# Optimization experiments

Measured on AMD Instinct MI355X. Metric: run time of the kernel, lower is better.

## Reference

```python
import jax, jax.numpy as jnp
import numpy as np

BN_EPS = 1e-5
NUM_ROUTING_ITERS = 3


def _bn(x, gamma, beta, axes):
    # training-mode batch norm (torch default train mode): batch statistics
    mean = x.mean(axes, keepdims=True)
    var = x.var(axes, keepdims=True)
    return (x - mean) * jax.lax.rsqrt(var + BN_EPS) * gamma + beta


def _squash(x):
    # squash over last dim: sn * x / ((1+sn) * sqrt(sn))
    sn = jnp.sum(x * x, axis=-1, keepdims=True)
    return sn * x / ((1.0 + sn) * jnp.sqrt(sn))


def setup_inputs() -> dict:
    key = jax.random.key(0)
    ks = jax.random.split(key, 16)
    B, N = 4, 2048          # batch, num_points
    P, Q = 1024, 16         # prim_caps_size, prim_vec_size
    L, V = 64, 64           # latent_caps_size, latent_vec_size
    OUT = 40
    s = 0.02
    return {
        "x": jax.random.normal(ks[0], (B, 3, N), dtype=jnp.float32),
        # ConvLayer
        "w1": jax.random.normal(ks[1], (64, 3), dtype=jnp.float32) * s,
        "b1": jnp.zeros((64,), jnp.float32),
        "g1": jnp.ones((64,), jnp.float32),
        "be1": jnp.zeros((64,), jnp.float32),
        "w2": jax.random.normal(ks[2], (128, 64), dtype=jnp.float32) * s,
        "b2": jnp.zeros((128,), jnp.float32),
        "g2": jnp.ones((128,), jnp.float32),
        "be2": jnp.zeros((128,), jnp.float32),
        # PrimaryPointCapsLayer: Q parallel conv1d(128->P, k=1)+BN branches, stacked
        "w3": jax.random.normal(ks[3], (Q, P, 128), dtype=jnp.float32) * s,
        "b3": jnp.zeros((Q, P), jnp.float32),
        "g3": jnp.ones((Q, P), jnp.float32),
        "be3": jnp.zeros((Q, P), jnp.float32),
        # LatentCapsLayer routing weights
        "Wr": jax.random.normal(ks[4], (L, P, V, Q), dtype=jnp.float32) * 0.01,
        # classifier head
        "fc_w": jax.random.normal(ks[5], (OUT, L * V), dtype=jnp.float32) * s,
        "fc_b": jnp.zeros((OUT,), jnp.float32),
    }


def reference(x, w1, b1, g1, be1, w2, b2, g2, be2, w3, b3, g3, be3, Wr, fc_w, fc_b):
    B = x.shape[0]
    # ConvLayer: two 1x1 conv1d + BN + ReLU
    h = jnp.einsum("oc,bcn->bon", w1, x) + b1[None, :, None]
    h = jax.nn.relu(_bn(h, g1[None, :, None], be1[None, :, None], (0, 2)))
    h = jnp.einsum("oc,bcn->bon", w2, h) + b2[None, :, None]
    h = jax.nn.relu(_bn(h, g2[None, :, None], be2[None, :, None], (0, 2)))  # [B,128,N]

    # PrimaryPointCapsLayer: Q branches of conv1d+BN+global maxpool, vectorized
    u = jnp.einsum("qpc,bcn->bqpn", w3, h) + b3[None, :, :, None]  # [B,Q,P,N]
    u = _bn(u, g3[None, :, :, None], be3[None, :, :, None], (0, 3))
    u = u.max(axis=-1)                      # global maxpool -> [B,Q,P]
    u = jnp.transpose(u, (0, 2, 1))         # stack dim=2 in torch -> [B,P,Q]
    u = _squash(u)                          # squash over prim_vec

    # LatentCapsLayer dynamic routing
    u_hat = jnp.einsum("lpvq,bpq->blpv", Wr, u)   # [B,L,P,V]
    u_hat_d = jax.lax.stop_gradient(u_hat)
    L, P = Wr.shape[0], Wr.shape[1]
    b_ij = jnp.zeros((B, L, P), u_hat.dtype)
    for _ in range(NUM_ROUTING_ITERS - 1):
        c_ij = jax.nn.softmax(b_ij, axis=1)
        v_j = _squash(jnp.einsum("blp,blpv->blv", c_ij, u_hat_d))
        b_ij = b_ij + jnp.einsum("blv,blpv->blp", v_j, u_hat_d)
    c_ij = jax.nn.softmax(b_ij, axis=1)
    v_j = _squash(jnp.einsum("blp,blpv->blv", c_ij, u_hat))  # [B,L,V]

    presence = jnp.linalg.norm(v_j, axis=2)                   # [B,L]
    logits = v_j.reshape(B, -1) @ fc_w.T + fc_b               # [B,OUT]
    return (logits, presence)
```

## Files before the change

kernel.cpp:

```cpp
#include <hip/hip_runtime.h>
#include <math.h>

#define BN_EPS 1e-5f

typedef __attribute__((ext_vector_type(8))) _Float16 half8;
typedef __attribute__((ext_vector_type(4))) float f32x4;
#define SPLIT_S  2048.0f
#define INV_S    (1.0f/2048.0f)

__global__ void k_conv1(const float* __restrict__ x, const float* __restrict__ w1,
                        float* __restrict__ y1) {
    int i = blockIdx.x * 256 + threadIdx.x;
    int o = i >> 11;
    int bn4 = (i & 2047) * 4;
    int b = bn4 >> 11, n = bn4 & 2047;
    const float* xb = x + (size_t)b * 6144 + n;
    float4 x0 = *(const float4*)(xb);
    float4 x1 = *(const float4*)(xb + 2048);
    float4 x2 = *(const float4*)(xb + 4096);
    float wa = w1[o*3+0], wb = w1[o*3+1], wc = w1[o*3+2];
    float4 r;
    r.x = wa*x0.x + wb*x1.x + wc*x2.x;
    r.y = wa*x0.y + wb*x1.y + wc*x2.y;
    r.z = wa*x0.z + wb*x1.z + wc*x2.z;
    r.w = wa*x0.w + wb*x1.w + wc*x2.w;
    *(float4*)(y1 + o * 8192 + bn4) = r;
}

__global__ void k_stats(const float* __restrict__ y, float* __restrict__ mean,
                        float* __restrict__ inv) {
    int c = blockIdx.x, t = threadIdx.x;
    float s = 0.f, ss = 0.f;
    const float4* src = (const float4*)(y + c * 8192);
    for (int i = t; i < 2048; i += 256) {
        float4 v = src[i];
        s += v.x + v.y + v.z + v.w;
        ss = fmaf(v.x, v.x, fmaf(v.y, v.y, fmaf(v.z, v.z, fmaf(v.w, v.w, ss))));
    }
    __shared__ float rs[256], rss[256];
    rs[t] = s; rss[t] = ss;
    __syncthreads();
    for (int off = 128; off > 0; off >>= 1) {
        if (t < off) { rs[t] += rs[t+off]; rss[t] += rss[t+off]; }
        __syncthreads();
    }
    if (t == 0) {
        float m = rs[0] * (1.f/8192.f);
        float var = rss[0] * (1.f/8192.f) - m*m;
        mean[c] = m;
        inv[c]  = rsqrtf(var + BN_EPS);
    }
}

__global__ void k_bnrelu(const float* __restrict__ y, float* __restrict__ h,
                         const float* __restrict__ mean, const float* __restrict__ inv,
                         const float* __restrict__ g, const float* __restrict__ be, int total4) {
    int i = blockIdx.x * 256 + threadIdx.x;
    if (i >= total4) return;
    int c = i >> 11;
    float sc = inv[c] * g[c], sh = be[c] - mean[c] * sc;
    float4 v = *(const float4*)(y + i * 4);
    v.x = fmaxf(fmaf(v.x, sc, sh), 0.f);
    v.y = fmaxf(fmaf(v.y, sc, sh), 0.f);
    v.z = fmaxf(fmaf(v.z, sc, sh), 0.f);
    v.w = fmaxf(fmaf(v.w, sc, sh), 0.f);
    *(float4*)(h + i * 4) = v;
}

__global__ __launch_bounds__(256) void k_conv2(const float* __restrict__ h1,
                                               const float* __restrict__ w2,
                                               float* __restrict__ y2) {
    int bn0 = (blockIdx.x * 256 + threadIdx.x) * 4;
    int og0 = blockIdx.y * 4;
    float4 acc[4];
#pragma unroll
    for (int j = 0; j < 4; ++j) acc[j] = float4{0.f,0.f,0.f,0.f};
    for (int c = 0; c < 64; ++c) {
        float4 hv = *(const float4*)(h1 + c*8192 + bn0);
#pragma unroll
        for (int j = 0; j < 4; ++j) {
            float w = w2[(og0+j)*64 + c];
            acc[j].x = fmaf(w, hv.x, acc[j].x); acc[j].y = fmaf(w, hv.y, acc[j].y);
            acc[j].z = fmaf(w, hv.z, acc[j].z); acc[j].w = fmaf(w, hv.w, acc[j].w);
        }
    }
#pragma unroll
    for (int j = 0; j < 4; ++j) *(float4*)(y2 + (og0+j)*8192 + bn0) = acc[j];
}

__global__ void k_split_w3(const float* __restrict__ w, _Float16* __restrict__ hi,
                           _Float16* __restrict__ lo) {
    int base = blockIdx.x * 256 + threadIdx.x;
#pragma unroll
    for (int it = 0; it < 4; ++it) {
        int i = (base + it * 131072) * 4;
        float4 d = *reinterpret_cast<const float4*>(w + i);
        float vs[4] = {d.x, d.y, d.z, d.w};
#pragma unroll
        for (int j = 0; j < 4; ++j) {
            _Float16 h = (_Float16)vs[j];
            hi[i + j] = h;
            lo[i + j] = (_Float16)((vs[j] - (float)h) * SPLIT_S);
        }
    }
}

__global__ __launch_bounds__(256) void k_h2t_split(const float* __restrict__ y2,
        const float* __restrict__ mean, const float* __restrict__ inv,
        const float* __restrict__ g, const float* __restrict__ be,
        _Float16* __restrict__ hi, _Float16* __restrict__ lo) {
    __shared__ float tile[64][65];
    const int t = threadIdx.x;
    const int bn0 = blockIdx.x * 64, c0 = blockIdx.y * 64;
#pragma unroll
    for (int r = 0; r < 16; ++r) {
        int idx = r * 256 + t;
        int cl = idx >> 6, bnl = idx & 63;
        int c = c0 + cl;
        float v = y2[(size_t)c * 8192 + bn0 + bnl];
        v = (v - mean[c]) * inv[c] * g[c] + be[c];
        tile[cl][bnl] = v > 0.f ? v : 0.f;
    }
    __syncthreads();
#pragma unroll
    for (int r = 0; r < 16; ++r) {
        int idx = r * 256 + t;
        int bnl = idx >> 6, cl = idx & 63;
        float v = tile[cl][bnl];
        _Float16 h = (_Float16)v;
        size_t o = (size_t)(bn0 + bnl) * 128 + c0 + cl;
        hi[o] = h;
        lo[o] = (_Float16)((v - (float)h) * SPLIT_S);
    }
}

__global__ __launch_bounds__(256, 2) void k_caps(
        const _Float16* __restrict__ w3h, const _Float16* __restrict__ w3l,
        const _Float16* __restrict__ h2h, const _Float16* __restrict__ h2l,
        float* __restrict__ umax, float* __restrict__ umin,
        float* __restrict__ usum_b, float* __restrict__ usumsq_b) {
    const int lane = threadIdx.x & 63, wave = threadIdx.x >> 6;
    const int b = blockIdx.y;
    const int mrow = blockIdx.x * 128 + wave * 32;
    const int r16 = lane & 15, kq = lane >> 4;

    __shared__ _Float16 Bs[2][8][64][8];

    half8 Ah[2][4], Al[2][4];
#pragma unroll
    for (int mt = 0; mt < 2; ++mt) {
        const size_t base = (size_t)(mrow + mt*16 + r16) * 128 + kq * 8;
#pragma unroll
        for (int ks = 0; ks < 4; ++ks) {
            Ah[mt][ks] = *reinterpret_cast<const half8*>(w3h + base + ks*32);
            Al[mt][ks] = *reinterpret_cast<const half8*>(w3l + base + ks*32);
        }
    }
    float mx[2][4], mn[2][4], sm[2][4], sq[2][4];
#pragma unroll
    for (int mt = 0; mt < 2; ++mt)
#pragma unroll
        for (int r = 0; r < 4; ++r) {
            mx[mt][r] = -3.4e38f; mn[mt][r] = 3.4e38f; sm[mt][r] = 0.f; sq[mt][r] = 0.f;
        }

    const int u0 = wave * 2;
    const int ks0 = u0 >> 1;
    const size_t srow = (size_t)(b*2048 + r16) * 128 + ks0 * 32 + kq * 8;

    {
        *reinterpret_cast<half8*>(&Bs[0][u0  ][lane][0]) = *reinterpret_cast<const half8*>(h2h + srow);
        *reinterpret_cast<half8*>(&Bs[0][u0+1][lane][0]) = *reinterpret_cast<const half8*>(h2l + srow);
    }
    __syncthreads();

    for (int nt = 0; nt < 128; ++nt) {
        const int buf = nt & 1;
        const int ntn = (nt + 1 < 128) ? nt + 1 : nt;
        const size_t snext = srow + (size_t)ntn * 16 * 128;
        half8 g0 = *reinterpret_cast<const half8*>(h2h + snext);
        half8 g1 = *reinterpret_cast<const half8*>(h2l + snext);

        f32x4 acc[2], accx[2];
#pragma unroll
        for (int mt = 0; mt < 2; ++mt) { acc[mt] = f32x4{0.f,0.f,0.f,0.f}; accx[mt] = f32x4{0.f,0.f,0.f,0.f}; }
#pragma unroll
        for (int ks = 0; ks < 4; ++ks) {
            half8 Bh = *reinterpret_cast<const half8*>(&Bs[buf][ks*2  ][lane][0]);
            half8 Bl = *reinterpret_cast<const half8*>(&Bs[buf][ks*2+1][lane][0]);
#pragma unroll
            for (int mt = 0; mt < 2; ++mt) {
                acc[mt]  = __builtin_amdgcn_mfma_f32_16x16x32_f16(Ah[mt][ks], Bh, acc[mt], 0, 0, 0);
                accx[mt] = __builtin_amdgcn_mfma_f32_16x16x32_f16(Ah[mt][ks], Bl, accx[mt], 0, 0, 0);
                accx[mt] = __builtin_amdgcn_mfma_f32_16x16x32_f16(Al[mt][ks], Bh, accx[mt], 0, 0, 0);
            }
        }
#pragma unroll
        for (int mt = 0; mt < 2; ++mt)
#pragma unroll
            for (int r = 0; r < 4; ++r) {
                float v = fmaf(accx[mt][r], INV_S, acc[mt][r]);
                mx[mt][r] = fmaxf(mx[mt][r], v);
                mn[mt][r] = fminf(mn[mt][r], v);
                sm[mt][r] += v;
                sq[mt][r] = fmaf(v, v, sq[mt][r]);
            }
        *reinterpret_cast<half8*>(&Bs[buf^1][u0  ][lane][0]) = g0;
        *reinterpret_cast<half8*>(&Bs[buf^1][u0+1][lane][0]) = g1;
        __syncthreads();
    }

#pragma unroll
    for (int off = 8; off >= 1; off >>= 1)
#pragma unroll
        for (int mt = 0; mt < 2; ++mt)
#pragma unroll
            for (int r = 0; r < 4; ++r) {
                mx[mt][r] = fmaxf(mx[mt][r], __shfl_xor(mx[mt][r], off));
                mn[mt][r] = fminf(mn[mt][r], __shfl_xor(mn[mt][r], off));
                sm[mt][r] += __shfl_xor(sm[mt][r], off);
                sq[mt][r] += __shfl_xor(sq[mt][r], off);
            }
    if (r16 == 0) {
#pragma unroll
        for (int mt = 0; mt < 2; ++mt)
#pragma unroll
            for (int r = 0; r < 4; ++r) {
                int qp = mrow + mt*16 + kq*4 + r;
                umax[b*16384 + qp]     = mx[mt][r];
                umin[b*16384 + qp]     = mn[mt][r];
                usum_b[b*16384 + qp]   = sm[mt][r];
                usumsq_b[b*16384 + qp] = sq[mt][r];
            }
    }
}

__global__ void k_u(const float* __restrict__ umax, const float* __restrict__ umin,
                    const float* __restrict__ usum_b, const float* __restrict__ usumsq_b,
                    const float* __restrict__ g3, const float* __restrict__ be3,
                    float* __restrict__ u) {
    int tg = blockIdx.x * 256 + threadIdx.x;
    int b = tg >> 10, p = tg & 1023;
    float ub[16]; float sn = 0.f;
#pragma unroll
    for (int q = 0; q < 16; ++q) {
        int qp = q * 1024 + p;
        float s  = usum_b[qp] + usum_b[16384+qp] + usum_b[32768+qp] + usum_b[49152+qp];
        float ss = usumsq_b[qp] + usumsq_b[16384+qp] + usumsq_b[32768+qp] + usumsq_b[49152+qp];
        float mean  = s * (1.f/8192.f);
        float var   = ss * (1.f/8192.f) - mean*mean;
        float scale = g3[qp] * rsqrtf(var + BN_EPS);
        float val = (scale >= 0.f) ? umax[b*16384 + qp] : umin[b*16384 + qp];
        float vb = (val - mean) * scale + be3[qp];
        ub[q] = vb; sn = fmaf(vb, vb, sn);
    }
    float f = sqrtf(sn) / (1.f + sn);
#pragma unroll
    for (int q = 0; q < 16; ++q) u[tg*16 + q] = ub[q] * f;
}

__global__ __launch_bounds__(256) void k_uhat(const float* __restrict__ Wr,
                                              const float* __restrict__ u,
                                              float* __restrict__ uhat) {
    const int t = threadIdx.x;
    const int l = blockIdx.y;
    __shared__ float wr[4][16][68];
    __shared__ float us[4][4][16];
    const int bb = t >> 6, v = t & 63;
    for (int sub = 0; sub < 8; ++sub) {
        const int p0 = blockIdx.x * 32 + sub * 4;
        const float* src = Wr + ((size_t)l * 1024 + p0) * 1024;
        if (sub) __syncthreads();
#pragma unroll
        for (int it = 0; it < 4; ++it) {
            float4 d = *(const float4*)(src + (it*256 + t) * 4);
            int vv = t >> 2, q0 = (t & 3) * 4;
            wr[it][q0  ][vv] = d.x; wr[it][q0+1][vv] = d.y;
            wr[it][q0+2][vv] = d.z; wr[it][q0+3][vv] = d.w;
        }
        {
            int p = t >> 6, b2 = (t >> 4) & 3, q = t & 15;
            us[p][b2][q] = u[((size_t)b2 * 1024 + p0 + p) * 16 + q];
        }
        __syncthreads();
#pragma unroll
        for (int p = 0; p < 4; ++p) {
            float acc = 0.f;
#pragma unroll
            for (int q = 0; q < 16; ++q) acc = fmaf(wr[p][q][v], us[p][bb][q], acc);
            uhat[((size_t)(bb * 64 + l) * 1024 + p0 + p) * 64 + v] = acc;
        }
    }
}

__global__ void k_passA(const float* __restrict__ uhat, float* __restrict__ vout) {
    const int t = threadIdx.x;
    const int c4 = t & 15, pr = t >> 4;
    const float* base = uhat + (size_t)blockIdx.x * 65536;
    float4 acc = float4{0.f,0.f,0.f,0.f};
    for (int it = 0; it < 64; ++it) {
        float4 d = *(const float4*)(base + (pr + it*16) * 64 + c4 * 4);
        acc.x += d.x; acc.y += d.y; acc.z += d.z; acc.w += d.w;
    }
    __shared__ float red[16][68];
    *(float4*)&red[pr][c4 * 4] = acc;
    __syncthreads();
    if (t < 64) {
        float s = 0.f;
#pragma unroll
        for (int w = 0; w < 16; ++w) s += red[w][t];
        s *= (1.f/64.f);
        float sn = s * s;
#pragma unroll
        for (int off = 32; off >= 1; off >>= 1) sn += __shfl_xor(sn, off);
        vout[blockIdx.x * 64 + t] = s * sqrtf(sn) / (1.f + sn);
    }
}

__global__ __launch_bounds__(256) void k_route(const float* __restrict__ uhat,
                                               const float* __restrict__ vin,
                                               float* __restrict__ bij,
                                               float* __restrict__ part, const int read_b) {
    const int blk = blockIdx.x;
    const int b = blk >> 7, ch = blk & 127;
    const int p0 = ch * 8;
    const int t = threadIdx.x;
    const int v = t & 63, w = t >> 6;
    __shared__ float uh[64][68];
    __shared__ float vs[64][68];
    __shared__ float bl[64];
    __shared__ float cl[64];
    {
        const float* src = vin + b * 4096;
        for (int i = t; i < 1024; i += 256) {
            float4 d = *(const float4*)(src + i * 4);
            int l = i >> 4, v0 = (i & 15) * 4;
            vs[l][v0] = d.x; vs[l][v0+1] = d.y; vs[l][v0+2] = d.z; vs[l][v0+3] = d.w;
        }
    }
    float sacc[16];
#pragma unroll
    for (int j = 0; j < 16; ++j) sacc[j] = 0.f;

    for (int pp = 0; pp < 8; ++pp) {
        const int p = p0 + pp;
        __syncthreads();
        const float* src = uhat + (size_t)b * 4194304 + (size_t)p * 64;
        for (int i = t; i < 1024; i += 256) {
            int l = i >> 4, v0 = (i & 15) * 4;
            float4 d = *(const float4*)(src + (size_t)l * 65536 + v0);
            uh[l][v0] = d.x; uh[l][v0+1] = d.y; uh[l][v0+2] = d.z; uh[l][v0+3] = d.w;
        }
        __syncthreads();
#pragma unroll
        for (int i = 0; i < 16; ++i) {
            const int l = w * 16 + i;
            float prod = uh[l][v] * vs[l][v];
#pragma unroll
            for (int off = 32; off >= 1; off >>= 1) prod += __shfl_xor(prod, off);
            if (v == 0) {
                float bb = prod;
                if (read_b) bb += bij[(b * 64 + l) * 1024 + p];
                bl[l] = bb;
                if (!read_b) bij[(b * 64 + l) * 1024 + p] = bb;
            }
        }
        __syncthreads();
        if (w == 0) {
            float xv = bl[v];
            float m = xv;
#pragma unroll
            for (int off = 32; off >= 1; off >>= 1) m = fmaxf(m, __shfl_xor(m, off));
            float e = expf(xv - m);
            float sgm = e;
#pragma unroll
            for (int off = 32; off >= 1; off >>= 1) sgm += __shfl_xor(sgm, off);
            cl[v] = e / sgm;
        }
        __syncthreads();
#pragma unroll
        for (int j = 0; j < 16; ++j) {
            const int l = j * 4 + w;
            sacc[j] = fmaf(cl[l], uh[l][v], sacc[j]);
        }
    }
#pragma unroll
    for (int j = 0; j < 16; ++j) {
        const int l = j * 4 + w;
        part[((size_t)(b * 128 + ch) * 64 + l) * 64 + v] = sacc[j];
    }
}

__global__ void k_red_squash(const float* __restrict__ part, float* __restrict__ vout,
                             float* __restrict__ pres) {
    const int wv = blockIdx.x;
    const int b = wv >> 6, l = wv & 63;
    const int v = threadIdx.x;
    float acc = 0.f;
    for (int ch = 0; ch < 128; ++ch) acc += part[((size_t)(b * 128 + ch) * 64 + l) * 64 + v];
    float sn = acc * acc;
#pragma unroll
    for (int off = 32; off >= 1; off >>= 1) sn += __shfl_xor(sn, off);
    vout[wv * 64 + v] = acc * sqrtf(sn) / (1.f + sn);
    if (pres != nullptr && v == 0) pres[wv] = sn / (1.f + sn);
}

__global__ void k_logits(const float* __restrict__ vj, const float* __restrict__ fcw,
                         const float* __restrict__ fcb, float* __restrict__ out) {
    int wv = blockIdx.x * 4 + (threadIdx.x >> 6);
    int lane = threadIdx.x & 63;
    int b = wv / 40, o = wv % 40;
    const float* xv = vj + b * 4096;
    const float* wr = fcw + (size_t)o * 4096;
    float acc = 0.f;
    for (int i = lane; i < 4096; i += 64) acc = fmaf(xv[i], wr[i], acc);
#pragma unroll
    for (int off = 32; off >= 1; off >>= 1) acc += __shfl_xor(acc, off);
    if (lane == 0) out[b * 40 + o] = acc + fcb[o];
}

extern "C" void kernel_launch(void* const* d_in, const int* in_sizes, int n_in,
                              void* d_out, int out_size, void* d_ws, size_t ws_size,
                              hipStream_t stream) {
    const float* x   = (const float*)d_in[0];
    const float* w1  = (const float*)d_in[1];
    const float* g1  = (const float*)d_in[3];
    const float* be1 = (const float*)d_in[4];
    const float* w2  = (const float*)d_in[5];
    const float* g2  = (const float*)d_in[7];
    const float* be2 = (const float*)d_in[8];
    const float* w3  = (const float*)d_in[9];
    const float* g3  = (const float*)d_in[11];
    const float* be3 = (const float*)d_in[12];
    const float* Wr  = (const float*)d_in[13];
    const float* fcw = (const float*)d_in[14];
    const float* fcb = (const float*)d_in[15];
    float* out = (float*)d_out;

    float* ws       = (float*)d_ws;
    float* y1       = ws;
    float* y2       = y1 + 524288;
    float* mean1    = y2 + 1048576;
    float* inv1     = mean1 + 64;
    float* mean2    = inv1 + 64;
    float* inv2     = mean2 + 128;
    float* umax     = inv2 + 128;
    float* umin     = umax + 65536;
    float* usum_b   = umin + 65536;
    float* usumsq_b = usum_b + 65536;
    float* u        = usumsq_b + 65536;
    float* v1       = u + 65536;
    float* v2       = v1 + 16384;
    float* vj       = v2 + 16384;
    float* bij      = vj + 16384;
    float* part     = bij + 262144;
    float* uhat     = part + 2097152;
    _Float16* w3h = (_Float16*)uhat;
    _Float16* w3l = w3h + 2097152;
    _Float16* h2h = w3l + 2097152;
    _Float16* h2l = h2h + 1048576;

    k_conv1<<<512, 256, 0, stream>>>(x, w1, y1);
    k_stats<<<64, 256, 0, stream>>>(y1, mean1, inv1);
    k_bnrelu<<<512, 256, 0, stream>>>(y1, y1, mean1, inv1, g1, be1, 131072);
    k_conv2<<<dim3(8, 32), 256, 0, stream>>>(y1, w2, y2);
    k_stats<<<128, 256, 0, stream>>>(y2, mean2, inv2);
    k_split_w3<<<512, 256, 0, stream>>>(w3, w3h, w3l);
    k_h2t_split<<<dim3(128, 2), 256, 0, stream>>>(y2, mean2, inv2, g2, be2, h2h, h2l);
    k_caps<<<dim3(128, 4), 256, 0, stream>>>(w3h, w3l, h2h, h2l, umax, umin, usum_b, usumsq_b);
    k_u<<<16, 256, 0, stream>>>(umax, umin, usum_b, usumsq_b, g3, be3, u);
    k_uhat<<<dim3(32, 64), 256, 0, stream>>>(Wr, u, uhat);
    k_passA<<<256, 256, 0, stream>>>(uhat, v1);
    k_route<<<512, 256, 0, stream>>>(uhat, v1, bij, part, 0);
    k_red_squash<<<256, 64, 0, stream>>>(part, v2, nullptr);
    k_route<<<512, 256, 0, stream>>>(uhat, v2, bij, part, 1);
    k_red_squash<<<256, 64, 0, stream>>>(part, vj, out + 160);
    k_logits<<<40, 256, 0, stream>>>(vj, fcw, fcb, out);
}
```

Measured before the change: 709.1 us.

## Fuse conv1 with stats and BN into conv2, transpose uhat, widen caps tiles

Conv1 now computes its BN statistics in the same kernel. The BN+ReLU step is folded into conv2's input load, which removes two launches and one full pass over y1. The caps kernel processes two 16-column N tiles per loop iteration with a doubled shared buffer, halving the number of barriers. uhat is stored in a [B,P,L,V] layout so route reads contiguous 16KB blocks, and the first routing pass's column sums come from partials accumulated in k_uhat, which drops the separate passA read of uhat. The costs are more LDS in k_caps and a new 2MB partial buffer plus its reduction kernel.

Result: faster. 694.2 us (-2.1%).

```diff
diff --git a/kernel.cpp b/kernel.cpp
--- a/kernel.cpp
+++ b/kernel.cpp
@@ -8,23 +8,42 @@
 #define SPLIT_S  2048.0f
 #define INV_S    (1.0f/2048.0f)
 
-__global__ void k_conv1(const float* __restrict__ x, const float* __restrict__ w1,
-                        float* __restrict__ y1) {
-    int i = blockIdx.x * 256 + threadIdx.x;
-    int o = i >> 11;
-    int bn4 = (i & 2047) * 4;
-    int b = bn4 >> 11, n = bn4 & 2047;
-    const float* xb = x + (size_t)b * 6144 + n;
-    float4 x0 = *(const float4*)(xb);
-    float4 x1 = *(const float4*)(xb + 2048);
-    float4 x2 = *(const float4*)(xb + 4096);
-    float wa = w1[o*3+0], wb = w1[o*3+1], wc = w1[o*3+2];
-    float4 r;
-    r.x = wa*x0.x + wb*x1.x + wc*x2.x;
-    r.y = wa*x0.y + wb*x1.y + wc*x2.y;
-    r.z = wa*x0.z + wb*x1.z + wc*x2.z;
-    r.w = wa*x0.w + wb*x1.w + wc*x2.w;
-    *(float4*)(y1 + o * 8192 + bn4) = r;
+__global__ __launch_bounds__(256) void k_conv1stats(const float* __restrict__ x,
+        const float* __restrict__ w1, float* __restrict__ y1,
+        float* __restrict__ mean, float* __restrict__ inv) {
+    const int o = blockIdx.x, t = threadIdx.x;
+    const float wa = w1[o*3+0], wb = w1[o*3+1], wc = w1[o*3+2];
+    float s = 0.f, ss = 0.f;
+#pragma unroll
+    for (int it = 0; it < 8; ++it) {
+        int i = it * 256 + t;
+        int b = i >> 9, n4 = (i & 511) * 4;
+        const float* xb = x + (size_t)b * 6144 + n4;
+        float4 x0 = *(const float4*)(xb);
+        float4 x1 = *(const float4*)(xb + 2048);
+        float4 x2 = *(const float4*)(xb + 4096);
+        float4 r;
+        r.x = wa*x0.x + wb*x1.x + wc*x2.x;
+        r.y = wa*x0.y + wb*x1.y + wc*x2.y;
+        r.z = wa*x0.z + wb*x1.z + wc*x2.z;
+        r.w = wa*x0.w + wb*x1.w + wc*x2.w;
+        *(float4*)(y1 + o * 8192 + i * 4) = r;
+        s += r.x + r.y + r.z + r.w;
+        ss = fmaf(r.x, r.x, fmaf(r.y, r.y, fmaf(r.z, r.z, fmaf(r.w, r.w, ss))));
+    }
+    __shared__ float rs[256], rss[256];
+    rs[t] = s; rss[t] = ss;
+    __syncthreads();
+    for (int off = 128; off > 0; off >>= 1) {
+        if (t < off) { rs[t] += rs[t+off]; rss[t] += rss[t+off]; }
+        __syncthreads();
+    }
+    if (t == 0) {
+        float m = rs[0] * (1.f/8192.f);
+        float var = rss[0] * (1.f/8192.f) - m*m;
+        mean[o] = m;
+        inv[o]  = rsqrtf(var + BN_EPS);
+    }
 }
 
 __global__ void k_stats(const float* __restrict__ y, float* __restrict__ mean,
@@ -52,31 +71,31 @@
     }
 }
 
-__global__ void k_bnrelu(const float* __restrict__ y, float* __restrict__ h,
-                         const float* __restrict__ mean, const float* __restrict__ inv,
-                         const float* __restrict__ g, const float* __restrict__ be, int total4) {
-    int i = blockIdx.x * 256 + threadIdx.x;
-    if (i >= total4) return;
-    int c = i >> 11;
-    float sc = inv[c] * g[c], sh = be[c] - mean[c] * sc;
-    float4 v = *(const float4*)(y + i * 4);
-    v.x = fmaxf(fmaf(v.x, sc, sh), 0.f);
-    v.y = fmaxf(fmaf(v.y, sc, sh), 0.f);
-    v.z = fmaxf(fmaf(v.z, sc, sh), 0.f);
-    v.w = fmaxf(fmaf(v.w, sc, sh), 0.f);
-    *(float4*)(h + i * 4) = v;
-}
-
-__global__ __launch_bounds__(256) void k_conv2(const float* __restrict__ h1,
-                                               const float* __restrict__ w2,
-                                               float* __restrict__ y2) {
-    int bn0 = (blockIdx.x * 256 + threadIdx.x) * 4;
+__global__ __launch_bounds__(256) void k_conv2(const float* __restrict__ y1,
+        const float* __restrict__ w2,
+        const float* __restrict__ mean1, const float* __restrict__ inv1,
+        const float* __restrict__ g1, const float* __restrict__ be1,
+        float* __restrict__ y2) {
+    __shared__ float sc1[64], sh1[64];
+    const int t = threadIdx.x;
+    if (t < 64) {
+        float sc = inv1[t] * g1[t];
+        sc1[t] = sc;
+        sh1[t] = be1[t] - mean1[t] * sc;
+    }
+    __syncthreads();
+    int bn0 = (blockIdx.x * 256 + t) * 4;
     int og0 = blockIdx.y * 4;
     float4 acc[4];
 #pragma unroll
     for (int j = 0; j < 4; ++j) acc[j] = float4{0.f,0.f,0.f,0.f};
     for (int c = 0; c < 64; ++c) {
-        float4 hv = *(const float4*)(h1 + c*8192 + bn0);
+        float4 hv = *(const float4*)(y1 + c*8192 + bn0);
+        float sc = sc1[c], sh = sh1[c];
+        hv.x = fmaxf(fmaf(hv.x, sc, sh), 0.f);
+        hv.y = fmaxf(fmaf(hv.y, sc, sh), 0.f);
+        hv.z = fmaxf(fmaf(hv.z, sc, sh), 0.f);
+        hv.w = fmaxf(fmaf(hv.w, sc, sh), 0.f);
 #pragma unroll
         for (int j = 0; j < 4; ++j) {
             float w = w2[(og0+j)*64 + c];
@@ -144,7 +163,7 @@
     const int mrow = blockIdx.x * 128 + wave * 32;
     const int r16 = lane & 15, kq = lane >> 4;
 
-    __shared__ _Float16 Bs[2][8][64][8];
+    __shared__ _Float16 Bs[2][2][8][64][8];
 
     half8 Ah[2][4], Al[2][4];
 #pragma unroll
@@ -165,48 +184,58 @@
         }
 
     const int u0 = wave * 2;
-    const int ks0 = u0 >> 1;
-    const size_t srow = (size_t)(b*2048 + r16) * 128 + ks0 * 32 + kq * 8;
+    const size_t srow = (size_t)(b*2048 + r16) * 128 + wave * 32 + kq * 8;
 
     {
-        *reinterpret_cast<half8*>(&Bs[0][u0  ][lane][0]) = *reinterpret_cast<const half8*>(h2h + srow);
-        *reinterpret_cast<half8*>(&Bs[0][u0+1][lane][0]) = *reinterpret_cast<const half8*>(h2l + srow);
+#pragma unroll
+        for (int g = 0; g < 2; ++g) {
+            const size_t a = srow + (size_t)g * 16 * 128;
+            *reinterpret_cast<half8*>(&Bs[0][g][u0  ][lane][0]) = *reinterpret_cast<const half8*>(h2h + a);
+            *reinterpret_cast<half8*>(&Bs[0][g][u0+1][lane][0]) = *reinterpret_cast<const half8*>(h2l + a);
+        }
     }
     __syncthreads();
 
-    for (int nt = 0; nt < 128; ++nt) {
+    for (int nt = 0; nt < 64; ++nt) {
         const int buf = nt & 1;
-        const int ntn = (nt + 1 < 128) ? nt + 1 : nt;
-        const size_t snext = srow + (size_t)ntn * 16 * 128;
-        half8 g0 = *reinterpret_cast<const half8*>(h2h + snext);
-        half8 g1 = *reinterpret_cast<const half8*>(h2l + snext);
-
-        f32x4 acc[2], accx[2];
-#pragma unroll
-        for (int mt = 0; mt < 2; ++mt) { acc[mt] = f32x4{0.f,0.f,0.f,0.f}; accx[mt] = f32x4{0.f,0.f,0.f,0.f}; }
-#pragma unroll
-        for (int ks = 0; ks < 4; ++ks) {
-            half8 Bh = *reinterpret_cast<const half8*>(&Bs[buf][ks*2  ][lane][0]);
-            half8 Bl = *reinterpret_cast<const half8*>(&Bs[buf][ks*2+1][lane][0]);
-#pragma unroll
-            for (int mt = 0; mt < 2; ++mt) {
-                acc[mt]  = __builtin_amdgcn_mfma_f32_16x16x32_f16(Ah[mt][ks], Bh, acc[mt], 0, 0, 0);
-                accx[mt] = __builtin_amdgcn_mfma_f32_16x16x32_f16(Ah[mt][ks], Bl, accx[mt], 0, 0, 0);
-                accx[mt] = __builtin_amdgcn_mfma_f32_16x16x32_f16(Al[mt][ks], Bh, accx[mt], 0, 0, 0);
+        const int ntn = (nt + 1 < 64) ? nt + 1 : nt;
+        const size_t snext = srow + (size_t)ntn * 32 * 128;
+        half8 g0h = *reinterpret_cast<const half8*>(h2h + snext);
+        half8 g0l = *reinterpret_cast<const half8*>(h2l + snext);
+        half8 g1h = *reinterpret_cast<const half8*>(h2h + snext + 2048);
+        half8 g1l = *reinterpret_cast<const half8*>(h2l + snext + 2048);
+
+#pragma unroll
+        for (int g = 0; g < 2; ++g) {
+            f32x4 acc[2], accx[2];
+#pragma unroll
+            for (int mt = 0; mt < 2; ++mt) { acc[mt] = f32x4{0.f,0.f,0.f,0.f}; accx[mt] = f32x4{0.f,0.f,0.f,0.f}; }
+#pragma unroll
+            for (int ks = 0; ks < 4; ++ks) {
+                half8 Bh = *reinterpret_cast<const half8*>(&Bs[buf][g][ks*2  ][lane][0]);
+                half8 Bl = *reinterpret_cast<const half8*>(&Bs[buf][g][ks*2+1][lane][0]);
+#pragma unroll
+                for (int mt = 0; mt < 2; ++mt) {
+                    acc[mt]  = __builtin_amdgcn_mfma_f32_16x16x32_f16(Ah[mt][ks], Bh, acc[mt], 0, 0, 0);
+                    accx[mt] = __builtin_amdgcn_mfma_f32_16x16x32_f16(Ah[mt][ks], Bl, accx[mt], 0, 0, 0);
+                    accx[mt] = __builtin_amdgcn_mfma_f32_16x16x32_f16(Al[mt][ks], Bh, accx[mt], 0, 0, 0);
+                }
             }
-        }
-#pragma unroll
-        for (int mt = 0; mt < 2; ++mt)
-#pragma unroll
-            for (int r = 0; r < 4; ++r) {
-                float v = fmaf(accx[mt][r], INV_S, acc[mt][r]);
-                mx[mt][r] = fmaxf(mx[mt][r], v);
-                mn[mt][r] = fminf(mn[mt][r], v);
-                sm[mt][r] += v;
-                sq[mt][r] = fmaf(v, v, sq[mt][r]);
-            }
-        *reinterpret_cast<half8*>(&Bs[buf^1][u0  ][lane][0]) = g0;
-        *reinterpret_cast<half8*>(&Bs[buf^1][u0+1][lane][0]) = g1;
+#pragma unroll
+            for (int mt = 0; mt < 2; ++mt)
+#pragma unroll
+                for (int r = 0; r < 4; ++r) {
+                    float v = fmaf(accx[mt][r], INV_S, acc[mt][r]);
+                    mx[mt][r] = fmaxf(mx[mt][r], v);
+                    mn[mt][r] = fminf(mn[mt][r], v);
+                    sm[mt][r] += v;
+                    sq[mt][r] = fmaf(v, v, sq[mt][r]);
+                }
+        }
+        *reinterpret_cast<half8*>(&Bs[buf^1][0][u0  ][lane][0]) = g0h;
+        *reinterpret_cast<half8*>(&Bs[buf^1][0][u0+1][lane][0]) = g0l;
+        *reinterpret_cast<half8*>(&Bs[buf^1][1][u0  ][lane][0]) = g1h;
+        *reinterpret_cast<half8*>(&Bs[buf^1][1][u0+1][lane][0]) = g1l;
         __syncthreads();
     }
 
@@ -261,14 +290,16 @@
 
 __global__ __launch_bounds__(256) void k_uhat(const float* __restrict__ Wr,
                                               const float* __restrict__ u,
-                                              float* __restrict__ uhat) {
+                                              float* __restrict__ uhat2,
+                                              float* __restrict__ s1p) {
     const int t = threadIdx.x;
-    const int l = blockIdx.y;
+    const int pblk = blockIdx.x, l = blockIdx.y;
     __shared__ float wr[4][16][68];
     __shared__ float us[4][4][16];
     const int bb = t >> 6, v = t & 63;
+    float s1acc = 0.f;
     for (int sub = 0; sub < 8; ++sub) {
-        const int p0 = blockIdx.x * 32 + sub * 4;
+        const int p0 = pblk * 32 + sub * 4;
         const float* src = Wr + ((size_t)l * 1024 + p0) * 1024;
         if (sub) __syncthreads();
 #pragma unroll
@@ -288,36 +319,29 @@
             float acc = 0.f;
 #pragma unroll
             for (int q = 0; q < 16; ++q) acc = fmaf(wr[p][q][v], us[p][bb][q], acc);
-            uhat[((size_t)(bb * 64 + l) * 1024 + p0 + p) * 64 + v] = acc;
-        }
-    }
-}
-
-__global__ void k_passA(const float* __restrict__ uhat, float* __restrict__ vout) {
-    const int t = threadIdx.x;
-    const int c4 = t & 15, pr = t >> 4;
-    const float* base = uhat + (size_t)blockIdx.x * 65536;
-    float4 acc = float4{0.f,0.f,0.f,0.f};
-    for (int it = 0; it < 64; ++it) {
-        float4 d = *(const float4*)(base + (pr + it*16) * 64 + c4 * 4);
-        acc.x += d.x; acc.y += d.y; acc.z += d.z; acc.w += d.w;
-    }
-    __shared__ float red[16][68];
-    *(float4*)&red[pr][c4 * 4] = acc;
-    __syncthreads();
-    if (t < 64) {
-        float s = 0.f;
-#pragma unroll
-        for (int w = 0; w < 16; ++w) s += red[w][t];
-        s *= (1.f/64.f);
-        float sn = s * s;
-#pragma unroll
-        for (int off = 32; off >= 1; off >>= 1) sn += __shfl_xor(sn, off);
-        vout[blockIdx.x * 64 + t] = s * sqrtf(sn) / (1.f + sn);
-    }
-}
-
-__global__ __launch_bounds__(256) void k_route(const float* __restrict__ uhat,
+            uhat2[(((size_t)bb * 1024 + p0 + p) * 64 + l) * 64 + v] = acc;
+            s1acc += acc;
+        }
+    }
+    s1p[(((size_t)pblk * 4 + bb) * 64 + l) * 64 + v] = s1acc;
+}
+
+__global__ void k_s1red(const float* __restrict__ s1p, float* __restrict__ vout) {
+    const int wv = blockIdx.x;
+    const int b = wv >> 6, l = wv & 63;
+    const int v = threadIdx.x;
+    float acc = 0.f;
+#pragma unroll
+    for (int pblk = 0; pblk < 32; ++pblk)
+        acc += s1p[(((size_t)pblk * 4 + b) * 64 + l) * 64 + v];
+    float s = acc * (1.f/64.f);
+    float sn = s * s;
+#pragma unroll
+    for (int off = 32; off >= 1; off >>= 1) sn += __shfl_xor(sn, off);
+    vout[wv * 64 + v] = s * sqrtf(sn) / (1.f + sn);
+}
+
+__global__ __launch_bounds__(256) void k_route(const float* __restrict__ uhat2,
                                                const float* __restrict__ vin,
                                                float* __restrict__ bij,
                                                float* __restrict__ part, const int read_b) {
@@ -345,10 +369,10 @@
     for (int pp = 0; pp < 8; ++pp) {
         const int p = p0 + pp;
         __syncthreads();
-        const float* src = uhat + (size_t)b * 4194304 + (size_t)p * 64;
+        const float* src = uhat2 + ((size_t)b * 1024 + p) * 4096;
         for (int i = t; i < 1024; i += 256) {
+            float4 d = *(const float4*)(src + i * 4);
             int l = i >> 4, v0 = (i & 15) * 4;
-            float4 d = *(const float4*)(src + (size_t)l * 65536 + v0);
             uh[l][v0] = d.x; uh[l][v0+1] = d.y; uh[l][v0+2] = d.z; uh[l][v0+3] = d.w;
         }
         __syncthreads();
@@ -453,27 +477,26 @@
     float* v2       = v1 + 16384;
     float* vj       = v2 + 16384;
     float* bij      = vj + 16384;
-    float* part     = bij + 262144;
-    float* uhat     = part + 2097152;
-    _Float16* w3h = (_Float16*)uhat;
+    float* s1p      = bij + 262144;
+    float* part     = s1p + 524288;
+    float* uhat2    = part + 2097152;
+    _Float16* w3h = (_Float16*)uhat2;
     _Float16* w3l = w3h + 2097152;
     _Float16* h2h = w3l + 2097152;
     _Float16* h2l = h2h + 1048576;
 
-    k_conv1<<<512, 256, 0, stream>>>(x, w1, y1);
-    k_stats<<<64, 256, 0, stream>>>(y1, mean1, inv1);
-    k_bnrelu<<<512, 256, 0, stream>>>(y1, y1, mean1, inv1, g1, be1, 131072);
-    k_conv2<<<dim3(8, 32), 256, 0, stream>>>(y1, w2, y2);
+    k_conv1stats<<<64, 256, 0, stream>>>(x, w1, y1, mean1, inv1);
+    k_conv2<<<dim3(8, 32), 256, 0, stream>>>(y1, w2, mean1, inv1, g1, be1, y2);
     k_stats<<<128, 256, 0, stream>>>(y2, mean2, inv2);
     k_split_w3<<<512, 256, 0, stream>>>(w3, w3h, w3l);
     k_h2t_split<<<dim3(128, 2), 256, 0, stream>>>(y2, mean2, inv2, g2, be2, h2h, h2l);
     k_caps<<<dim3(128, 4), 256, 0, stream>>>(w3h, w3l, h2h, h2l, umax, umin, usum_b, usumsq_b);
     k_u<<<16, 256, 0, stream>>>(umax, umin, usum_b, usumsq_b, g3, be3, u);
-    k_uhat<<<dim3(32, 64), 256, 0, stream>>>(Wr, u, uhat);
-    k_passA<<<256, 256, 0, stream>>>(uhat, v1);
-    k_route<<<512, 256, 0, stream>>>(uhat, v1, bij, part, 0);
+    k_uhat<<<dim3(32, 64), 256, 0, stream>>>(Wr, u, uhat2, s1p);
+    k_s1red<<<256, 64, 0, stream>>>(s1p, v1);
+    k_route<<<512, 256, 0, stream>>>(uhat2, v1, bij, part, 0);
     k_red_squash<<<256, 64, 0, stream>>>(part, v2, nullptr);
-    k_route<<<512, 256, 0, stream>>>(uhat, v2, bij, part, 1);
+    k_route<<<512, 256, 0, stream>>>(uhat2, v2, bij, part, 1);
     k_red_squash<<<256, 64, 0, stream>>>(part, vj, out + 160);
     k_logits<<<40, 256, 0, stream>>>(vj, fcw, fcb, out);
 }
```
